# Performance work log

Hardware: AMD Instinct MI355X
Metric: run time of the kernel (lower is better)

## Reference

```python
import jax, jax.numpy as jnp
import numpy as np

B, S, D = 4, 2048, 512
QKD = 256
HID = 3 * D  # expansion_factor=3
EPS = 1e-5


def _ln(x, g, b):
    m = jnp.mean(x, axis=-1, keepdims=True)
    v = jnp.mean((x - m) ** 2, axis=-1, keepdims=True)
    return (x - m) * jax.lax.rsqrt(v + EPS) * g + b


def setup_inputs() -> dict:
    key = jax.random.key(0)
    ks = jax.random.split(key, 12)
    s = lambda fan: 1.0 / np.sqrt(fan)
    return {
        "x":  jax.random.normal(ks[0], (B, S, D), jnp.float32),
        "Wm": jax.random.uniform(ks[1], (D, D), jnp.float32, -s(D), s(D)),
        "bm": jnp.zeros((D,), jnp.float32),
        "g1": jnp.ones((D,), jnp.float32),
        "b1": jnp.zeros((D,), jnp.float32),
        "Wh": jax.random.uniform(ks[2], (2 * HID, D), jnp.float32, -s(D), s(D)),
        "bh": jnp.zeros((2 * HID,), jnp.float32),
        "Wq": jax.random.uniform(ks[3], (QKD, D), jnp.float32, -s(D), s(D)),
        "bq": jnp.zeros((QKD,), jnp.float32),
        "Wb": jax.random.normal(ks[4], (QKD, QKD), jnp.float32),
        "Wo": jax.random.uniform(ks[5], (D, HID), jnp.float32, -s(HID), s(HID)),
        "bo": jnp.zeros((D,), jnp.float32),
        "g2": jnp.ones((D,), jnp.float32),
        "b2": jnp.zeros((D,), jnp.float32),
    }


def reference(x, Wm, bm, g1, b1, Wh, bh, Wq, bq, Wb, Wo, bo, g2, b2):
    seq_len = x.shape[-2]
    memory = jnp.einsum('bsd,ed->bse', x, Wm) + bm
    normed = _ln(x + memory, g1, b1)
    h = jax.nn.relu(jnp.einsum('bsd,hd->bsh', normed, Wh) + bh)
    v, gate = h[..., :HID], h[..., HID:]
    Z = jax.nn.relu(jnp.einsum('bsd,qd->bsq', normed, Wq) + bq)  # [B,S,QKD]
    QK = jnp.einsum('bid,de,bje->bij', Z, Wb, Z) / seq_len
    A = jax.nn.relu(QK) ** 2  # relu^2 attention, no softmax
    V = jnp.einsum('bij,bjd->bid', A, v) * gate
    out = _ln(jnp.einsum('bsh,dh->bsd', V, Wo) + bo, g2, b2)
    return out + x
```

## Files before the change

### kernel.cpp

```cpp
#include <hip/hip_runtime.h>

typedef unsigned short u16;
typedef unsigned char u8;
typedef __attribute__((ext_vector_type(8))) short short8;
typedef __attribute__((ext_vector_type(4))) float f32x4;

#define LN_EPS 1e-5f
#define SCALE_A 4096.f
#define SCALE_V 8.f
#define INV_SCALE_AV (1.f/32768.f)

__device__ __forceinline__ u16 f2bf(float f){
    union { float f; unsigned u; } c; c.f = f;
    unsigned u = c.u + 0x7FFFu + ((c.u >> 16) & 1u);
    return (u16)(u >> 16);
}
__device__ __forceinline__ float bf2f(u16 h){
    union { unsigned u; float f; } c; c.u = ((unsigned)h) << 16;
    return c.f;
}
__device__ __forceinline__ u8 f2fp8(float f){
    int r = __builtin_amdgcn_cvt_pk_fp8_f32(f, 0.f, 0, false);
    return (u8)(r & 0xFF);
}

enum { EPI_NONE=0, EPI_BIAS_RES, EPI_BIAS_RELU, EPI_RELUSQ, EPI_GATE, EPI_BIAS, EPI_HSPLIT };
enum { OT_F32=0, OT_BF16=1, OT_FP8=2 };

__device__ __forceinline__ void gl2lds16(const void* g, void* lds){
    __builtin_amdgcn_global_load_lds(
        (const __attribute__((address_space(1))) unsigned*)g,
        (__attribute__((address_space(3))) unsigned*)lds, 16, 0, 0);
}

template<int EPI, int OT>
__global__ __launch_bounds__(256)
void mgemm(const u16* __restrict__ A, const u16* __restrict__ B, void* __restrict__ Cv,
           int K, int lda, int ldb, int ldc,
           long sAb, long sBb, long sCb,
           const float* __restrict__ bias,
           const void* __restrict__ ext, int ldext, long sEb,
           float scale, u16* __restrict__ out2, int hsplit)
{
    __shared__ u16 sA[4096];
    __shared__ u16 sB[4096];
    const int tid = threadIdx.x;
    const int m0 = blockIdx.y * 128, n0 = blockIdx.x * 128;
    const int z  = blockIdx.z;
    const u16* Az = A + (size_t)z * sAb;
    const u16* Bz = B + (size_t)z * sBb;

    const int lane = tid & 63, quad = lane >> 4, l15 = lane & 15;
    const int wave = tid >> 6;
    const int wm = (wave >> 1) * 64, wn = (wave & 1) * 64;

    const u16* gA[2]; const u16* gB[2]; int lo[2];
#pragma unroll
    for (int r = 0; r < 2; r++){
        const int c = tid + r * 256;
        gA[r] = Az + (size_t)(m0 + (c & 127)) * lda + (c >> 7) * 8;
        gB[r] = Bz + (size_t)(n0 + (c & 127)) * ldb + (c >> 7) * 8;
        lo[r] = ((tid & 192) + r * 256) * 16;
    }

    f32x4 acc[4][4];
#pragma unroll
    for (int i = 0; i < 4; i++)
#pragma unroll
        for (int j = 0; j < 4; j++) acc[i][j] = (f32x4){0.f,0.f,0.f,0.f};

    const u16* fA = sA + quad * 1024 + (wm + l15) * 8;
    const u16* fB = sB + quad * 1024 + (wn + l15) * 8;

    for (int k0 = 0; k0 < K; k0 += 32){
#pragma unroll
        for (int r = 0; r < 2; r++){
            gl2lds16(gA[r] + k0, (char*)sA + lo[r]);
            gl2lds16(gB[r] + k0, (char*)sB + lo[r]);
        }
        __syncthreads();
        short8 a[4], b[4];
#pragma unroll
        for (int t = 0; t < 4; t++){
            a[t] = *(const short8*)(fA + t * 128);
            b[t] = *(const short8*)(fB + t * 128);
        }
#pragma unroll
        for (int i = 0; i < 4; i++)
#pragma unroll
            for (int j = 0; j < 4; j++)
                acc[i][j] = __builtin_amdgcn_mfma_f32_16x16x32_bf16(a[i], b[j], acc[i][j], 0, 0, 0);
        __syncthreads();
    }

    float* Cf = (float*)Cv; u16* Ch = (u16*)Cv; u8* C8 = (u8*)Cv;
    const size_t zc = (size_t)z * sCb;
#pragma unroll
    for (int i = 0; i < 4; i++){
#pragma unroll
        for (int j = 0; j < 4; j++){
            const int n = n0 + wn + j * 16 + l15;
            float bs = 0.f;
            if (EPI==EPI_BIAS_RES || EPI==EPI_BIAS_RELU || EPI==EPI_BIAS || EPI==EPI_HSPLIT)
                bs = bias[n];
#pragma unroll
            for (int r = 0; r < 4; r++){
                const int m = m0 + wm + i * 16 + quad * 4 + r;
                float v = acc[i][j][r] + bs;
                if (EPI==EPI_BIAS_RES)
                    v += ((const float*)ext)[(size_t)m * ldext + n];
                if (EPI==EPI_BIAS_RELU || EPI==EPI_HSPLIT)
                    v = fmaxf(v, 0.f);
                if (EPI==EPI_RELUSQ){ float t = fmaxf(v * scale, 0.f); v = t * t * SCALE_A; }
                if (EPI==EPI_GATE)
                    v *= bf2f(((const u16*)ext)[(size_t)z * sEb + (size_t)m * ldext + n]);
                if (EPI==EPI_HSPLIT){
                    if (n < hsplit){
                        if (OT==OT_FP8) C8[(size_t)m * ldc + n] = f2fp8(v * SCALE_V);
                        else            Ch[(size_t)m * ldc + n] = f2bf(v);
                    } else {
                        out2[(size_t)m * ldc + n - hsplit] = f2bf(v);
                    }
                } else if (OT==OT_FP8){
                    C8[zc + (size_t)m * ldc + n] = f2fp8(v);
                } else if (OT==OT_BF16){
                    Ch[zc + (size_t)m * ldc + n] = f2bf(v);
                } else {
                    Cf[zc + (size_t)m * ldc + n] = v;
                }
            }
        }
    }
}

__global__ __launch_bounds__(256)
void mgemm8(const u8* __restrict__ A, const u8* __restrict__ B, u16* __restrict__ C,
            int K, int lda, int ldb, int ldc,
            long sAb, long sBb, long sCb,
            const u16* __restrict__ gate, int ldext, long sEb)
{
    __shared__ u8 sA[4096];
    __shared__ u8 sB[4096];
    const int tid = threadIdx.x;
    const int m0 = blockIdx.y * 128, n0 = blockIdx.x * 128;
    const int z  = blockIdx.z;
    const u8* Az = A + (size_t)z * sAb;
    const u8* Bz = B + (size_t)z * sBb;

    const int lane = tid & 63, quad = lane >> 4, l15 = lane & 15;
    const int wave = tid >> 6;
    const int wm = (wave >> 1) * 64, wn = (wave & 1) * 64;

    const u8* gA = Az + (size_t)(m0 + (tid & 127)) * lda + (tid >> 7) * 16;
    const u8* gB = Bz + (size_t)(n0 + (tid & 127)) * ldb + (tid >> 7) * 16;
    const int lo = (tid & 192) * 16;

    f32x4 acc[4][4];
#pragma unroll
    for (int i = 0; i < 4; i++)
#pragma unroll
        for (int j = 0; j < 4; j++) acc[i][j] = (f32x4){0.f,0.f,0.f,0.f};

    const u8* fA = sA + (quad >> 1) * 2048 + (size_t)(wm + l15) * 16 + (quad & 1) * 8;
    const u8* fB = sB + (quad >> 1) * 2048 + (size_t)(wn + l15) * 16 + (quad & 1) * 8;

    for (int k0 = 0; k0 < K; k0 += 32){
        gl2lds16(gA + k0, (char*)sA + lo);
        gl2lds16(gB + k0, (char*)sB + lo);
        __syncthreads();
        long a[4], b[4];
#pragma unroll
        for (int t = 0; t < 4; t++){
            a[t] = *(const long*)(fA + t * 256);
            b[t] = *(const long*)(fB + t * 256);
        }
#pragma unroll
        for (int i = 0; i < 4; i++)
#pragma unroll
            for (int j = 0; j < 4; j++)
                acc[i][j] = __builtin_amdgcn_mfma_f32_16x16x32_fp8_fp8(a[i], b[j], acc[i][j], 0, 0, 0);
        __syncthreads();
    }

    const size_t zc = (size_t)z * sCb;
#pragma unroll
    for (int i = 0; i < 4; i++){
#pragma unroll
        for (int j = 0; j < 4; j++){
            const int n = n0 + wn + j * 16 + l15;
#pragma unroll
            for (int r = 0; r < 4; r++){
                const int m = m0 + wm + i * 16 + quad * 4 + r;
                float v = acc[i][j][r] * INV_SCALE_AV
                        * bf2f(gate[(size_t)z * sEb + (size_t)m * ldext + n]);
                C[zc + (size_t)m * ldc + n] = f2bf(v);
            }
        }
    }
}

template<bool OUT_BF, bool ADD_RES, bool SUM2>
__global__ __launch_bounds__(256)
void ln_k(const float* __restrict__ in, const float* __restrict__ g,
          const float* __restrict__ b, const float* __restrict__ res,
          const float* __restrict__ in2, const float* __restrict__ bias2,
          void* __restrict__ out)
{
    const int row = blockIdx.x, tid = threadIdx.x;
    float2 v = *(const float2*)(in + (size_t)row * 512 + tid * 2);
    if (SUM2){
        const float2 w = *(const float2*)(in2 + (size_t)row * 512 + tid * 2);
        const float2 bb2 = *(const float2*)(bias2 + tid * 2);
        v.x += w.x + bb2.x; v.y += w.y + bb2.y;
    }
    float s = v.x + v.y, ss = v.x * v.x + v.y * v.y;
#pragma unroll
    for (int off = 32; off > 0; off >>= 1){
        s  += __shfl_down(s,  off);
        ss += __shfl_down(ss, off);
    }
    __shared__ float sbuf[8], ssbuf[8];
    const int wid = tid >> 6, lane = tid & 63;
    if (lane == 0){ sbuf[wid] = s; ssbuf[wid] = ss; }
    __syncthreads();
    if (tid == 0){
        float S = 0.f, SS = 0.f;
#pragma unroll
        for (int i = 0; i < 4; i++){ S += sbuf[i]; SS += ssbuf[i]; }
        const float mean = S * (1.f/512.f);
        const float var  = SS * (1.f/512.f) - mean * mean;
        sbuf[4]  = mean;
        ssbuf[4] = rsqrtf(var + LN_EPS);
    }
    __syncthreads();
    const float mean = sbuf[4], rstd = ssbuf[4];
    const float2 gg = *(const float2*)(g + tid * 2);
    const float2 bb = *(const float2*)(b + tid * 2);
    float ox = (v.x - mean) * rstd * gg.x + bb.x;
    float oy = (v.y - mean) * rstd * gg.y + bb.y;
    if (ADD_RES){
        const float2 r = *(const float2*)(res + (size_t)row * 512 + tid * 2);
        ox += r.x; oy += r.y;
    }
    if (OUT_BF){
        unsigned pk = ((unsigned)f2bf(oy) << 16) | (unsigned)f2bf(ox);
        ((unsigned*)out)[(size_t)row * 256 + tid] = pk;
    } else {
        *(float2*)((float*)out + (size_t)row * 512 + tid * 2) = make_float2(ox, oy);
    }
}

__global__ __launch_bounds__(256)
void castall_k(const float* __restrict__ x, const float* __restrict__ Wm,
               const float* __restrict__ Wh, const float* __restrict__ Wq,
               const float* __restrict__ Wo,
               u16* __restrict__ xb, u16* __restrict__ Wmb, u16* __restrict__ Whb,
               u16* __restrict__ Wqb, u16* __restrict__ Wob)
{
    const int i = blockIdx.x * 256 + threadIdx.x;
    const float* src; u16* dst; int off;
    if      (i < 1048576){ src = x;  dst = xb;  off = i; }
    else if (i < 1114112){ src = Wm; dst = Wmb; off = i - 1048576; }
    else if (i < 1507328){ src = Wh; dst = Whb; off = i - 1114112; }
    else if (i < 1540096){ src = Wq; dst = Wqb; off = i - 1507328; }
    else if (i < 1736704){ src = Wo; dst = Wob; off = i - 1540096; }
    else return;
    const float4 v = ((const float4*)src)[off];
    ushort4 o; o.x = f2bf(v.x); o.y = f2bf(v.y); o.z = f2bf(v.z); o.w = f2bf(v.w);
    ((ushort4*)dst)[off] = o;
}

__global__ __launch_bounds__(256)
void wbt_k(const float* __restrict__ Wb, u16* __restrict__ WbT){
    int i = blockIdx.x * 256 + threadIdx.x;
    int e = i >> 8, d = i & 255;
    WbT[e * 256 + d] = f2bf(Wb[d * 256 + e]);
}

__global__ __launch_bounds__(256)
void tr8_k(const u8* __restrict__ v, u8* __restrict__ vT, int S, int HID){
    const int b = blockIdx.z;
    const int h0 = blockIdx.x * 64, s0 = blockIdx.y * 64;
    __shared__ u8 t[64][68];
    const u8* vb = v + (size_t)b * S * HID;
    u8* vTb = vT + (size_t)b * HID * S;
    const int tid = threadIdx.x;
#pragma unroll
    for (int i = 0; i < 4; i++){
        int idx = tid + i * 256;
        int r = idx >> 4, c4 = (idx & 15) * 4;
        uchar4 u = *(const uchar4*)(vb + (size_t)(s0 + r) * HID + h0 + c4);
        t[r][c4] = u.x; t[r][c4+1] = u.y; t[r][c4+2] = u.z; t[r][c4+3] = u.w;
    }
    __syncthreads();
#pragma unroll
    for (int i = 0; i < 4; i++){
        int idx = tid + i * 256;
        int r = idx >> 4, c4 = (idx & 15) * 4;
        uchar4 u;
        u.x = t[c4][r]; u.y = t[c4+1][r]; u.z = t[c4+2][r]; u.w = t[c4+3][r];
        *(uchar4*)(vTb + (size_t)(h0 + r) * S + s0 + c4) = u;
    }
}

extern "C" void kernel_launch(void* const* d_in, const int* in_sizes, int n_in,
                              void* d_out, int out_size, void* d_ws, size_t ws_size,
                              hipStream_t stream)
{
    const float* x  = (const float*)d_in[0];
    const float* Wm = (const float*)d_in[1];
    const float* bm = (const float*)d_in[2];
    const float* g1 = (const float*)d_in[3];
    const float* b1 = (const float*)d_in[4];
    const float* Wh = (const float*)d_in[5];
    const float* bh = (const float*)d_in[6];
    const float* Wq = (const float*)d_in[7];
    const float* bq = (const float*)d_in[8];
    const float* Wb = (const float*)d_in[9];
    const float* Wo = (const float*)d_in[10];
    const float* bo = (const float*)d_in[11];
    const float* g2 = (const float*)d_in[12];
    const float* b2 = (const float*)d_in[13];
    float* out = (float*)d_out;
    (void)in_sizes; (void)n_in; (void)out_size; (void)ws_size;

    const int Bn=4, S=2048, D=512, QKD=256, HID=1536, H2=3072;
    const int M = Bn * S;

    char* p = (char*)d_ws;
    auto alloc = [&](size_t bytes)->void*{ void* r = p; p += (bytes + 255) & ~(size_t)255; return r; };
    u16*  xbf  = (u16*) alloc((size_t)M*D*2);
    u16*  Wmbf = (u16*) alloc((size_t)D*D*2);
    u16*  Whbf = (u16*) alloc((size_t)H2*D*2);
    u16*  Wqbf = (u16*) alloc((size_t)QKD*D*2);
    u16*  Wobf = (u16*) alloc((size_t)D*HID*2);
    u16*  WbT  = (u16*) alloc((size_t)QKD*QKD*2);
    float* ybuf= (float*)alloc((size_t)M*D*4);
    float* ybuf2=(float*)alloc((size_t)M*D*4);
    u16*  Zb   = (u16*) alloc((size_t)M*QKD*2);
    u16*  ZWbb = (u16*) alloc((size_t)M*QKD*2);
    u8*   v8   = (u8*)  alloc((size_t)M*HID);
    u16*  gbf  = (u16*) alloc((size_t)M*HID*2);
    u8*   vT8  = (u8*)  alloc((size_t)M*HID);
    u8*   A8   = (u8*)  alloc((size_t)M*S);
    u16*  Vgbf = (u16*) alloc((size_t)M*HID*2);
    u16*  nrm  = xbf;

    dim3 blk(256);

    castall_k<<<dim3(6784), blk, 0, stream>>>(x, Wm, Wh, Wq, Wo, xbf, Wmbf, Whbf, Wqbf, Wobf);
    wbt_k<<<dim3(QKD*QKD/256), blk, 0, stream>>>(Wb, WbT);

    mgemm<EPI_BIAS_RES,OT_F32><<<dim3(D/128, M/128, 1), blk, 0, stream>>>(
        xbf, Wmbf, ybuf, D, D, D, D, 0,0,0, bm, x, D, 0, 1.f, nullptr, 0);
    ln_k<true,false,false><<<dim3(M), blk, 0, stream>>>(ybuf, g1, b1, nullptr, nullptr, nullptr, nrm);
    mgemm<EPI_HSPLIT,OT_FP8><<<dim3(H2/128, M/128, 1), blk, 0, stream>>>(
        nrm, Whbf, v8, D, D, D, HID, 0,0,0, bh, nullptr, 0, 0, 1.f, gbf, HID);
    mgemm<EPI_BIAS_RELU,OT_BF16><<<dim3(QKD/128, M/128, 1), blk, 0, stream>>>(
        nrm, Wqbf, Zb, D, D, D, QKD, 0,0,0, bq, nullptr, 0, 0, 1.f, nullptr, 0);
    mgemm<EPI_NONE,OT_BF16><<<dim3(QKD/128, M/128, 1), blk, 0, stream>>>(
        Zb, WbT, ZWbb, QKD, QKD, QKD, QKD, 0,0,0, nullptr, nullptr, 0, 0, 1.f, nullptr, 0);
    mgemm<EPI_RELUSQ,OT_FP8><<<dim3(S/128, S/128, Bn), blk, 0, stream>>>(
        ZWbb, Zb, A8, QKD, QKD, QKD, S,
        (long)S*QKD, (long)S*QKD, (long)S*S,
        nullptr, nullptr, 0, 0, 1.f/(float)S, nullptr, 0);
    tr8_k<<<dim3(HID/64, S/64, Bn), blk, 0, stream>>>(v8, vT8, S, HID);
    mgemm8<<<dim3(HID/128, S/128, Bn), blk, 0, stream>>>(
        A8, vT8, Vgbf, S, S, S, HID,
        (long)S*S, (long)HID*S, (long)S*HID,
        gbf, HID, (long)S*HID);
    mgemm<EPI_NONE,OT_F32><<<dim3(D/128, M/128, 2), blk, 0, stream>>>(
        Vgbf, Wobf, ybuf, HID/2, HID, HID, D,
        (long)HID/2, (long)HID/2, (long)M*D,
        nullptr, nullptr, 0, 0, 1.f, nullptr, 0);
    ln_k<false,true,true><<<dim3(M), blk, 0, stream>>>(ybuf, g2, b2, x, ybuf2, bo, out);
}
```

Measured before the change: 371.6 us.

## Double-buffer GEMM LDS staging, widen fp8 K-step, split-K memory and output GEMMs

Both GEMM kernels now stage the next K tile into a second LDS buffer while the current one is consumed. This drops one barrier per iteration and overlaps global loads with MFMA work. The fp8 GEMM also moves to a 64-wide K step per iteration. The memory GEMM becomes a 2-way split-K with bias and residual folded into the LayerNorm, and the output GEMM becomes 3-way split-K. The Wb transpose is merged into the cast kernel, which removes one launch. The costs are extra fp32 partial buffers and traffic, more LDS per block (which may reduce occupancy), and a single barrier per iteration that must still guard against buffer overwrite.

```diff
diff --git a/kernel.cpp b/kernel.cpp
--- a/kernel.cpp
+++ b/kernel.cpp
@@ -24,7 +24,7 @@
     return (u8)(r & 0xFF);
 }
 
-enum { EPI_NONE=0, EPI_BIAS_RES, EPI_BIAS_RELU, EPI_RELUSQ, EPI_GATE, EPI_BIAS, EPI_HSPLIT };
+enum { EPI_NONE=0, EPI_BIAS_RELU, EPI_RELUSQ, EPI_HSPLIT };
 enum { OT_F32=0, OT_BF16=1, OT_FP8=2 };
 
 __device__ __forceinline__ void gl2lds16(const void* g, void* lds){
@@ -42,8 +42,8 @@
            const void* __restrict__ ext, int ldext, long sEb,
            float scale, u16* __restrict__ out2, int hsplit)
 {
-    __shared__ u16 sA[4096];
-    __shared__ u16 sB[4096];
+    __shared__ u16 sA[2][4096];
+    __shared__ u16 sB[2][4096];
     const int tid = threadIdx.x;
     const int m0 = blockIdx.y * 128, n0 = blockIdx.x * 128;
     const int z  = blockIdx.z;
@@ -63,22 +63,27 @@
         lo[r] = ((tid & 192) + r * 256) * 16;
     }
 
+    auto stage = [&](int buf, int k0){
+#pragma unroll
+        for (int r = 0; r < 2; r++){
+            gl2lds16(gA[r] + k0, (char*)sA[buf] + lo[r]);
+            gl2lds16(gB[r] + k0, (char*)sB[buf] + lo[r]);
+        }
+    };
+
     f32x4 acc[4][4];
 #pragma unroll
     for (int i = 0; i < 4; i++)
 #pragma unroll
         for (int j = 0; j < 4; j++) acc[i][j] = (f32x4){0.f,0.f,0.f,0.f};
 
-    const u16* fA = sA + quad * 1024 + (wm + l15) * 8;
-    const u16* fB = sB + quad * 1024 + (wn + l15) * 8;
-
+    stage(0, 0);
+    int buf = 0;
     for (int k0 = 0; k0 < K; k0 += 32){
-#pragma unroll
-        for (int r = 0; r < 2; r++){
-            gl2lds16(gA[r] + k0, (char*)sA + lo[r]);
-            gl2lds16(gB[r] + k0, (char*)sB + lo[r]);
-        }
         __syncthreads();
+        if (k0 + 32 < K) stage(buf ^ 1, k0 + 32);
+        const u16* fA = sA[buf] + quad * 1024 + (wm + l15) * 8;
+        const u16* fB = sB[buf] + quad * 1024 + (wn + l15) * 8;
         short8 a[4], b[4];
 #pragma unroll
         for (int t = 0; t < 4; t++){
@@ -90,7 +95,7 @@
 #pragma unroll
             for (int j = 0; j < 4; j++)
                 acc[i][j] = __builtin_amdgcn_mfma_f32_16x16x32_bf16(a[i], b[j], acc[i][j], 0, 0, 0);
-        __syncthreads();
+        buf ^= 1;
     }
 
     float* Cf = (float*)Cv; u16* Ch = (u16*)Cv; u8* C8 = (u8*)Cv;
@@ -101,26 +106,16 @@
         for (int j = 0; j < 4; j++){
             const int n = n0 + wn + j * 16 + l15;
             float bs = 0.f;
-            if (EPI==EPI_BIAS_RES || EPI==EPI_BIAS_RELU || EPI==EPI_BIAS || EPI==EPI_HSPLIT)
-                bs = bias[n];
+            if (EPI==EPI_BIAS_RELU || EPI==EPI_HSPLIT) bs = bias[n];
 #pragma unroll
             for (int r = 0; r < 4; r++){
                 const int m = m0 + wm + i * 16 + quad * 4 + r;
                 float v = acc[i][j][r] + bs;
-                if (EPI==EPI_BIAS_RES)
-                    v += ((const float*)ext)[(size_t)m * ldext + n];
-                if (EPI==EPI_BIAS_RELU || EPI==EPI_HSPLIT)
-                    v = fmaxf(v, 0.f);
+                if (EPI==EPI_BIAS_RELU || EPI==EPI_HSPLIT) v = fmaxf(v, 0.f);
                 if (EPI==EPI_RELUSQ){ float t = fmaxf(v * scale, 0.f); v = t * t * SCALE_A; }
-                if (EPI==EPI_GATE)
-                    v *= bf2f(((const u16*)ext)[(size_t)z * sEb + (size_t)m * ldext + n]);
                 if (EPI==EPI_HSPLIT){
-                    if (n < hsplit){
-                        if (OT==OT_FP8) C8[(size_t)m * ldc + n] = f2fp8(v * SCALE_V);
-                        else            Ch[(size_t)m * ldc + n] = f2bf(v);
-                    } else {
-                        out2[(size_t)m * ldc + n - hsplit] = f2bf(v);
-                    }
+                    if (n < hsplit) C8[(size_t)m * ldc + n] = f2fp8(v * SCALE_V);
+                    else            out2[(size_t)m * ldc + n - hsplit] = f2bf(v);
                 } else if (OT==OT_FP8){
                     C8[zc + (size_t)m * ldc + n] = f2fp8(v);
                 } else if (OT==OT_BF16){
@@ -139,8 +134,8 @@
             long sAb, long sBb, long sCb,
             const u16* __restrict__ gate, int ldext, long sEb)
 {
-    __shared__ u8 sA[4096];
-    __shared__ u8 sB[4096];
+    __shared__ u8 sA[2][8192];
+    __shared__ u8 sB[2][8192];
     const int tid = threadIdx.x;
     const int m0 = blockIdx.y * 128, n0 = blockIdx.x * 128;
     const int z  = blockIdx.z;
@@ -151,9 +146,22 @@
     const int wave = tid >> 6;
     const int wm = (wave >> 1) * 64, wn = (wave & 1) * 64;
 
-    const u8* gA = Az + (size_t)(m0 + (tid & 127)) * lda + (tid >> 7) * 16;
-    const u8* gB = Bz + (size_t)(n0 + (tid & 127)) * ldb + (tid >> 7) * 16;
-    const int lo = (tid & 192) * 16;
+    const u8* gA[2]; const u8* gB[2]; int lo[2];
+#pragma unroll
+    for (int r = 0; r < 2; r++){
+        const int c = tid + r * 256;
+        gA[r] = Az + (size_t)(m0 + (c & 127)) * lda + (c >> 7) * 16;
+        gB[r] = Bz + (size_t)(n0 + (c & 127)) * ldb + (c >> 7) * 16;
+        lo[r] = ((tid & 192) + r * 256) * 16;
+    }
+
+    auto stage = [&](int buf, int k0){
+#pragma unroll
+        for (int r = 0; r < 2; r++){
+            gl2lds16(gA[r] + k0, (char*)sA[buf] + lo[r]);
+            gl2lds16(gB[r] + k0, (char*)sB[buf] + lo[r]);
+        }
+    };
 
     f32x4 acc[4][4];
 #pragma unroll
@@ -161,25 +169,28 @@
 #pragma unroll
         for (int j = 0; j < 4; j++) acc[i][j] = (f32x4){0.f,0.f,0.f,0.f};
 
-    const u8* fA = sA + (quad >> 1) * 2048 + (size_t)(wm + l15) * 16 + (quad & 1) * 8;
-    const u8* fB = sB + (quad >> 1) * 2048 + (size_t)(wn + l15) * 16 + (quad & 1) * 8;
-
-    for (int k0 = 0; k0 < K; k0 += 32){
-        gl2lds16(gA + k0, (char*)sA + lo);
-        gl2lds16(gB + k0, (char*)sB + lo);
+    stage(0, 0);
+    int buf = 0;
+    for (int k0 = 0; k0 < K; k0 += 64){
         __syncthreads();
-        long a[4], b[4];
-#pragma unroll
-        for (int t = 0; t < 4; t++){
-            a[t] = *(const long*)(fA + t * 256);
-            b[t] = *(const long*)(fB + t * 256);
-        }
-#pragma unroll
-        for (int i = 0; i < 4; i++)
-#pragma unroll
-            for (int j = 0; j < 4; j++)
-                acc[i][j] = __builtin_amdgcn_mfma_f32_16x16x32_fp8_fp8(a[i], b[j], acc[i][j], 0, 0, 0);
-        __syncthreads();
+        if (k0 + 64 < K) stage(buf ^ 1, k0 + 64);
+#pragma unroll
+        for (int t = 0; t < 2; t++){
+            const u8* fA = sA[buf] + t * 4096 + (quad >> 1) * 2048 + (wm + l15) * 16 + (quad & 1) * 8;
+            const u8* fB = sB[buf] + t * 4096 + (quad >> 1) * 2048 + (wn + l15) * 16 + (quad & 1) * 8;
+            long a[4], b[4];
+#pragma unroll
+            for (int q = 0; q < 4; q++){
+                a[q] = *(const long*)(fA + q * 256);
+                b[q] = *(const long*)(fB + q * 256);
+            }
+#pragma unroll
+            for (int i = 0; i < 4; i++)
+#pragma unroll
+                for (int j = 0; j < 4; j++)
+                    acc[i][j] = __builtin_amdgcn_mfma_f32_16x16x32_fp8_fp8(a[i], b[j], acc[i][j], 0, 0, 0);
+        }
+        buf ^= 1;
     }
 
     const size_t zc = (size_t)z * sCb;
@@ -199,19 +210,28 @@
     }
 }
 
-template<bool OUT_BF, bool ADD_RES, bool SUM2>
+template<bool OUT_BF, bool POST_RES, int NSUM, bool PRE_RES>
 __global__ __launch_bounds__(256)
 void ln_k(const float* __restrict__ in, const float* __restrict__ g,
-          const float* __restrict__ b, const float* __restrict__ res,
-          const float* __restrict__ in2, const float* __restrict__ bias2,
-          void* __restrict__ out)
+          const float* __restrict__ b, const float* __restrict__ res_post,
+          const float* __restrict__ res_pre, const float* __restrict__ bias2,
+          long pstride, void* __restrict__ out)
 {
     const int row = blockIdx.x, tid = threadIdx.x;
-    float2 v = *(const float2*)(in + (size_t)row * 512 + tid * 2);
-    if (SUM2){
-        const float2 w = *(const float2*)(in2 + (size_t)row * 512 + tid * 2);
+    const size_t base = (size_t)row * 512 + tid * 2;
+    float2 v = *(const float2*)(in + base);
+#pragma unroll
+    for (int p = 1; p < NSUM; p++){
+        const float2 w = *(const float2*)(in + (size_t)p * pstride + base);
+        v.x += w.x; v.y += w.y;
+    }
+    if (NSUM > 1){
         const float2 bb2 = *(const float2*)(bias2 + tid * 2);
-        v.x += w.x + bb2.x; v.y += w.y + bb2.y;
+        v.x += bb2.x; v.y += bb2.y;
+    }
+    if (PRE_RES){
+        const float2 r = *(const float2*)(res_pre + base);
+        v.x += r.x; v.y += r.y;
     }
     float s = v.x + v.y, ss = v.x * v.x + v.y * v.y;
 #pragma unroll
@@ -238,43 +258,43 @@
     const float2 bb = *(const float2*)(b + tid * 2);
     float ox = (v.x - mean) * rstd * gg.x + bb.x;
     float oy = (v.y - mean) * rstd * gg.y + bb.y;
-    if (ADD_RES){
-        const float2 r = *(const float2*)(res + (size_t)row * 512 + tid * 2);
+    if (POST_RES){
+        const float2 r = *(const float2*)(res_post + base);
         ox += r.x; oy += r.y;
     }
     if (OUT_BF){
         unsigned pk = ((unsigned)f2bf(oy) << 16) | (unsigned)f2bf(ox);
         ((unsigned*)out)[(size_t)row * 256 + tid] = pk;
     } else {
-        *(float2*)((float*)out + (size_t)row * 512 + tid * 2) = make_float2(ox, oy);
+        *(float2*)((float*)out + base) = make_float2(ox, oy);
     }
 }
 
 __global__ __launch_bounds__(256)
 void castall_k(const float* __restrict__ x, const float* __restrict__ Wm,
                const float* __restrict__ Wh, const float* __restrict__ Wq,
-               const float* __restrict__ Wo,
+               const float* __restrict__ Wo, const float* __restrict__ Wb,
                u16* __restrict__ xb, u16* __restrict__ Wmb, u16* __restrict__ Whb,
-               u16* __restrict__ Wqb, u16* __restrict__ Wob)
+               u16* __restrict__ Wqb, u16* __restrict__ Wob, u16* __restrict__ WbT)
 {
     const int i = blockIdx.x * 256 + threadIdx.x;
+    if (i >= 1736704){
+        const int j = i - 1736704;
+        if (j < 65536){
+            const int e = j >> 8, d = j & 255;
+            WbT[e * 256 + d] = f2bf(Wb[d * 256 + e]);
+        }
+        return;
+    }
     const float* src; u16* dst; int off;
     if      (i < 1048576){ src = x;  dst = xb;  off = i; }
     else if (i < 1114112){ src = Wm; dst = Wmb; off = i - 1048576; }
     else if (i < 1507328){ src = Wh; dst = Whb; off = i - 1114112; }
     else if (i < 1540096){ src = Wq; dst = Wqb; off = i - 1507328; }
-    else if (i < 1736704){ src = Wo; dst = Wob; off = i - 1540096; }
-    else return;
+    else                 { src = Wo; dst = Wob; off = i - 1540096; }
     const float4 v = ((const float4*)src)[off];
     ushort4 o; o.x = f2bf(v.x); o.y = f2bf(v.y); o.z = f2bf(v.z); o.w = f2bf(v.w);
     ((ushort4*)dst)[off] = o;
-}
-
-__global__ __launch_bounds__(256)
-void wbt_k(const float* __restrict__ Wb, u16* __restrict__ WbT){
-    int i = blockIdx.x * 256 + threadIdx.x;
-    int e = i >> 8, d = i & 255;
-    WbT[e * 256 + d] = f2bf(Wb[d * 256 + e]);
 }
 
 __global__ __launch_bounds__(256)
@@ -326,6 +346,7 @@
 
     const int Bn=4, S=2048, D=512, QKD=256, HID=1536, H2=3072;
     const int M = Bn * S;
+    const long MD = (long)M * D;
 
     char* p = (char*)d_ws;
     auto alloc = [&](size_t bytes)->void*{ void* r = p; p += (bytes + 255) & ~(size_t)255; return r; };
@@ -335,8 +356,7 @@
     u16*  Wqbf = (u16*) alloc((size_t)QKD*D*2);
     u16*  Wobf = (u16*) alloc((size_t)D*HID*2);
     u16*  WbT  = (u16*) alloc((size_t)QKD*QKD*2);
-    float* ybuf= (float*)alloc((size_t)M*D*4);
-    float* ybuf2=(float*)alloc((size_t)M*D*4);
+    float* ybuf= (float*)alloc((size_t)MD*4*3);
     u16*  Zb   = (u16*) alloc((size_t)M*QKD*2);
     u16*  ZWbb = (u16*) alloc((size_t)M*QKD*2);
     u8*   v8   = (u8*)  alloc((size_t)M*HID);
@@ -348,12 +368,13 @@
 
     dim3 blk(256);
 
-    castall_k<<<dim3(6784), blk, 0, stream>>>(x, Wm, Wh, Wq, Wo, xbf, Wmbf, Whbf, Wqbf, Wobf);
-    wbt_k<<<dim3(QKD*QKD/256), blk, 0, stream>>>(Wb, WbT);
-
-    mgemm<EPI_BIAS_RES,OT_F32><<<dim3(D/128, M/128, 1), blk, 0, stream>>>(
-        xbf, Wmbf, ybuf, D, D, D, D, 0,0,0, bm, x, D, 0, 1.f, nullptr, 0);
-    ln_k<true,false,false><<<dim3(M), blk, 0, stream>>>(ybuf, g1, b1, nullptr, nullptr, nullptr, nrm);
+    castall_k<<<dim3(7040), blk, 0, stream>>>(x, Wm, Wh, Wq, Wo, Wb,
+                                              xbf, Wmbf, Whbf, Wqbf, Wobf, WbT);
+    mgemm<EPI_NONE,OT_F32><<<dim3(D/128, M/128, 2), blk, 0, stream>>>(
+        xbf, Wmbf, ybuf, D/2, D, D, D, 256, 256, MD,
+        nullptr, nullptr, 0, 0, 1.f, nullptr, 0);
+    ln_k<true,false,2,true><<<dim3(M), blk, 0, stream>>>(
+        ybuf, g1, b1, nullptr, x, bm, MD, nrm);
     mgemm<EPI_HSPLIT,OT_FP8><<<dim3(H2/128, M/128, 1), blk, 0, stream>>>(
         nrm, Whbf, v8, D, D, D, HID, 0,0,0, bh, nullptr, 0, 0, 1.f, gbf, HID);
     mgemm<EPI_BIAS_RELU,OT_BF16><<<dim3(QKD/128, M/128, 1), blk, 0, stream>>>(
@@ -369,9 +390,9 @@
         A8, vT8, Vgbf, S, S, S, HID,
         (long)S*S, (long)HID*S, (long)S*HID,
         gbf, HID, (long)S*HID);
-    mgemm<EPI_NONE,OT_F32><<<dim3(D/128, M/128, 2), blk, 0, stream>>>(
-        Vgbf, Wobf, ybuf, HID/2, HID, HID, D,
-        (long)HID/2, (long)HID/2, (long)M*D,
+    mgemm<EPI_NONE,OT_F32><<<dim3(D/128, M/128, 3), blk, 0, stream>>>(
+        Vgbf, Wobf, ybuf, HID/3, HID, HID, D, 512, 512, MD,
         nullptr, nullptr, 0, 0, 1.f, nullptr, 0);
-    ln_k<false,true,true><<<dim3(M), blk, 0, stream>>>(ybuf, g2, b2, x, ybuf2, bo, out);
-}
+    ln_k<false,true,3,false><<<dim3(M), blk, 0, stream>>>(
+        ybuf, g2, b2, x, nullptr, bo, MD, out);
+}
```

After: 377.0 us. About the same (+1.4%).
